# Kernel optimization log

Measured on AMD Instinct MI355X. Metric: run time of the kernel, lower is better.

The kernel has to match this reference:

```python
import jax, jax.numpy as jnp
import numpy as np

D_M, L_OBS, ALPHA, D_H, D_V, N_HEADS = 64, 256, 256, 256, 64, 8


def setup_inputs():
    key = jax.random.key(0)
    ks = jax.random.split(key, 18)
    x_ts = jax.random.normal(ks[0], (D_M, L_OBS), dtype=jnp.float32)
    t_raw = jax.random.uniform(ks[1], (D_M, L_OBS), dtype=jnp.float32) * ALPHA
    drop = jax.random.uniform(ks[2], (D_M, L_OBS)) < 0.5
    t_ts = jnp.where(drop, -1.0, t_raw)  # negative time == invalid observation
    global_means = jax.random.normal(ks[3], (D_M,), dtype=jnp.float32)
    s = 0.05
    return {
        'x_ts': x_ts, 't_ts': t_ts, 'global_means': global_means,
        'conv_w': jax.random.normal(ks[4], (D_H, D_M)) * s,
        'conv_b': jax.random.normal(ks[5], (D_H,)) * s,
        't2v_w': jax.random.normal(ks[6], (N_HEADS, D_V)),
        't2v_phi': jax.random.normal(ks[7], (N_HEADS, D_V)),
        'wq_w': jax.random.normal(ks[8], (N_HEADS, D_V, D_V)) * s,
        'wq_b': jax.random.normal(ks[9], (N_HEADS, D_V)) * s,
        'wk_w': jax.random.normal(ks[10], (N_HEADS, D_V, D_V)) * s,
        'wk_b': jax.random.normal(ks[11], (N_HEADS, D_V)) * s,
        'proj_w': jax.random.normal(ks[12], (D_H, N_HEADS)) * s,
        'proj_b': jax.random.normal(ks[13], (D_H,)) * s,
        'g1_w': jax.random.normal(ks[14], (D_H, 2 * D_H)) * s,
        'g1_b': jax.random.normal(ks[15], (D_H,)) * s,
        'g2_w': jax.random.normal(ks[16], (D_H, D_H)) * s,
        'g2_b': jax.random.normal(ks[17], (D_H,)) * s,
    }


def _time2vec(tau, w, phi):
    # tau [...], w/phi [H, D_V] -> [H, *tau.shape, D_V]; dim 0 linear, rest sin
    shp = (N_HEADS,) + (1,) * tau.ndim + (D_V,)
    full = w.reshape(shp) * tau[None, ..., None] + phi.reshape(shp)
    return jnp.concatenate([full[..., :1], jnp.sin(full[..., 1:])], axis=-1)


def _impute_row(x, t, gm):
    # ALPHA grid via int(time), then forward-fill starting from global mean.
    valid = (~jnp.isnan(x)) & (t >= 0)
    idx = t.astype(jnp.int32)  # truncation matches int(obs_time.item()) for t>=0
    inr = valid & (idx < ALPHA)
    seg = jnp.where(inr, idx, ALPHA)  # invalid obs go to dropped segment
    order = jnp.arange(L_OBS, dtype=jnp.int32)
    last = jax.ops.segment_max(jnp.where(inr, order, -1), seg,
                               num_segments=ALPHA + 1)[:ALPHA]
    present = last >= 0
    vals = x[jnp.clip(last, 0, L_OBS - 1)]          # value written to each slot
    pos = jnp.where(present, jnp.arange(ALPHA, dtype=jnp.int32), -1)
    lastpos = jax.lax.cummax(pos, axis=0)            # last observed slot <= t
    return jnp.where(lastpos >= 0, vals[jnp.clip(lastpos, 0, ALPHA - 1)], gm)


def _forward(x_ts, t_ts, global_means, conv_w, conv_b, t2v_w, t2v_phi,
             wq_w, wq_b, wk_w, wk_b, proj_w, proj_b, g1_w, g1_b, g2_w, g2_b):
    # --- imputation branch ---
    regular = jax.vmap(_impute_row)(x_ts, t_ts, global_means)  # [d_m, alpha]
    e_imp = (conv_w @ regular).T + conv_b                      # [alpha, d_h]
    # --- mTAND branch (masked attention over ragged observations) ---
    valid = (~jnp.isnan(x_ts)) & (t_ts >= 0)                   # [d_m, L]
    x_safe = jnp.where(valid, x_ts, 0.0)
    t_safe = jnp.where(valid, t_ts, 0.0)
    alpha_pts = jnp.arange(ALPHA, dtype=jnp.float32)
    theta_a = _time2vec(alpha_pts, t2v_w, t2v_phi)             # [H, alpha, d_v]
    q = jnp.einsum('had,hed->hae', theta_a, wq_w) + wq_b[:, None, :]
    theta_o = _time2vec(t_safe, t2v_w, t2v_phi)                # [H, d_m, L, d_v]
    k = jnp.einsum('hjld,hed->hjle', theta_o, wk_w) + wk_b[:, None, None, :]
    scores = jnp.einsum('hae,hjle->hjal', q, k) / np.float32(np.sqrt(D_V))
    scores = jnp.where(valid[None, :, None, :], scores, -1e9)  # exp underflows to 0
    attn = jax.nn.softmax(scores, axis=-1)                     # [H, d_m, alpha, L]
    # fully-invalid features: uniform attn * x_safe==0 -> zeros (matches torch)
    interp = jnp.einsum('hjal,jl->jah', attn, x_safe)          # [d_m, alpha, H]
    e_attn = (interp @ proj_w.T + proj_b).mean(axis=0)         # [alpha, d_h]
    # --- hidden_space gate ---
    concat = jnp.concatenate([e_imp, e_attn], axis=-1)         # [alpha, 2*d_h]
    g = jax.nn.sigmoid(jax.nn.relu(concat @ g1_w.T + g1_b) @ g2_w.T + g2_b)
    return g * e_imp + (1.0 - g) * e_attn                      # [alpha, d_h]


def reference(x_ts, t_ts, global_means, conv_w, conv_b, t2v_w, t2v_phi,
              wq_w, wq_b, wk_w, wk_b, proj_w, proj_b, g1_w, g1_b, g2_w, g2_b):
    return _forward(x_ts, t_ts, global_means, conv_w, conv_b, t2v_w, t2v_phi,
                    wq_w, wq_b, wk_w, wk_b, proj_w, proj_b, g1_w, g1_b, g2_w, g2_b)
```

## Files before the change

kernel.cpp:

```cpp
#include <hip/hip_runtime.h>

#define D_M     64
#define L_OBS   256
#define ALPHA   256
#define D_H     256
#define D_V     64
#define N_HEADS 8

typedef _Float16 half8 __attribute__((ext_vector_type(8)));
typedef float    f32x4 __attribute__((ext_vector_type(4)));

__global__ __launch_bounds__(256) void prep_kernel(
    const float* __restrict__ x_ts, const float* __restrict__ t_ts,
    const float* __restrict__ gm,
    const float* __restrict__ t2v_w, const float* __restrict__ t2v_phi,
    const float* __restrict__ wq_w, const float* __restrict__ wq_b,
    const float* __restrict__ wk_w,
    float* __restrict__ regular, float* __restrict__ QWbuf,
    float* __restrict__ QWabsG)
{
    const int tid = threadIdx.x;

    __shared__ int   last[ALPHA];
    __shared__ float vals[ALPHA];
    __shared__ int   wtot[4];
    __shared__ __align__(16) float wq_s[D_V][68];
    __shared__ __align__(16) float thA[16][68];
    __shared__ __align__(16) float QaT[16][68];

    if (blockIdx.x < D_M) {
        const int m  = blockIdx.x;
        const int l  = tid;
        const int wv = tid >> 6;
        const int ln = tid & 63;
        last[l] = -1;
        __syncthreads();
        float x = x_ts[m * L_OBS + l];
        float t = t_ts[m * L_OBS + l];
        bool valid = (x == x) && (t >= 0.0f);
        int idx = (int)t;
        if (valid && idx < ALPHA) atomicMax(&last[idx], l);
        __syncthreads();
        int li = last[l];
        vals[l] = (li >= 0) ? x_ts[m * L_OBS + li] : 0.0f;
        int p = (li >= 0) ? l : -1;
        #pragma unroll
        for (int s = 1; s < 64; s <<= 1) {
            int q = __shfl_up(p, s);
            if (ln >= s && q > p) p = q;
        }
        if (ln == 63) wtot[wv] = p;
        __syncthreads();
        int pre = -1;
        for (int w = 0; w < 4; w++)
            if (w < wv && wtot[w] > pre) pre = wtot[w];
        int lp = (pre > p) ? pre : p;
        regular[m * ALPHA + l] = (lp >= 0) ? vals[lp] : gm[m];
    } else {
        const int pb = blockIdx.x - D_M;
        const int h  = pb >> 4;
        const int a0 = (pb & 15) * 16;

        {
            const float4* w4 = (const float4*)(wq_w + h * D_V * D_V);
            #pragma unroll
            for (int i = 0; i < 4; i++) {
                int f = i * 256 + tid;
                float4 v = w4[f];
                int e = f >> 4, c = (f & 15) * 4;
                *(float4*)&wq_s[e][c] = v;
            }
        }
        {
            int al = tid >> 4, j0 = (tid & 15) * 4;
            float tv = (float)(a0 + al);
            #pragma unroll
            for (int j = 0; j < 4; j++) {
                int d = j0 + j;
                float f = t2v_w[h * D_V + d] * tv + t2v_phi[h * D_V + d];
                thA[al][d] = (d == 0) ? f : __sinf(f);
            }
        }
        __syncthreads();

        {
            const int e  = tid >> 2;
            const int ap = tid & 3;
            float accA[4] = {0.f, 0.f, 0.f, 0.f};
            const float4* wrow = (const float4*)&wq_s[e][0];
            #pragma unroll
            for (int j = 0; j < 16; j++) {
                float4 w = wrow[j];
                #pragma unroll
                for (int k = 0; k < 4; k++) {
                    float4 tv = *(const float4*)&thA[ap + 4 * k][j * 4];
                    accA[k] += w.x * tv.x + w.y * tv.y + w.z * tv.z + w.w * tv.w;
                }
            }
            float bq = wq_b[h * D_V + e];
            #pragma unroll
            for (int k = 0; k < 4; k++) QaT[ap + 4 * k][e] = accA[k] + bq;
        }
        __syncthreads();

        const int d  = tid >> 2;
        const int ap = tid & 3;
        float accB[4] = {0.f, 0.f, 0.f, 0.f};
        #pragma unroll 4
        for (int e4 = 0; e4 < 16; e4++) {
            const float* wkp = &wk_w[(h * D_V + e4 * 4) * D_V + d];
            float w0 = wkp[0];
            float w1 = wkp[D_V];
            float w2 = wkp[2 * D_V];
            float w3 = wkp[3 * D_V];
            #pragma unroll
            for (int k = 0; k < 4; k++) {
                float4 qv = *(const float4*)&QaT[ap + 4 * k][e4 * 4];
                accB[k] += qv.x * w0 + qv.y * w1 + qv.z * w2 + qv.w * w3;
            }
        }
        #pragma unroll
        for (int k = 0; k < 4; k++)
            QWbuf[h * D_V * ALPHA + d * ALPHA + a0 + ap + 4 * k] = accB[k];

        __syncthreads();
        #pragma unroll
        for (int k = 0; k < 4; k++)
            wq_s[d][ap + 4 * k] = (d == 0) ? 0.0f : fabsf(accB[k]);
        __syncthreads();
        if (tid < 16) {
            float s = 0.0f;
            #pragma unroll 8
            for (int dd = 0; dd < D_V; dd++) s += wq_s[dd][tid];
            QWabsG[h * ALPHA + a0 + tid] = s;
        }
    }
}

__global__ __launch_bounds__(256) void attn_mfma_kernel(
    const float* __restrict__ x_ts, const float* __restrict__ t_ts,
    const float* __restrict__ t2v_w, const float* __restrict__ t2v_phi,
    const float* __restrict__ QWbuf, const float* __restrict__ QWabsG,
    float* __restrict__ interp)
{
    const int ah  = blockIdx.x;
    const int m   = blockIdx.y;
    const int h   = blockIdx.z;
    const int tid = threadIdx.x;
    const int wv  = tid >> 6;
    const int ln  = tid & 63;
    const int lg  = ln >> 4;
    const int lc  = ln & 15;

    __shared__ float xc[L_OBS], tc[L_OBS];
    __shared__ float w_sh[D_V], phi_sh[D_V];
    __shared__ __align__(16) _Float16 hiB[2][2048];
    __shared__ __align__(16) _Float16 reB[2][2048];
    __shared__ float red_s[8];
    __shared__ int   cnt_s[4];

    xc[tid] = 0.0f;
    tc[tid] = 0.0f;
    float x = x_ts[m * L_OBS + tid];
    float t = t_ts[m * L_OBS + tid];
    bool  v = (x == x) && (t >= 0.0f);
    unsigned long long bal = __ballot(v);
    if (ln == 0) cnt_s[wv] = __popcll(bal);
    {
        float tmx = v ? t : -3.0e38f;
        float tmn = v ? t : 3.0e38f;
        #pragma unroll
        for (int s = 1; s < 64; s <<= 1) {
            tmx = fmaxf(tmx, __shfl_xor(tmx, s));
            tmn = fminf(tmn, __shfl_xor(tmn, s));
        }
        if (ln == 0) { red_s[wv] = tmx; red_s[4 + wv] = tmn; }
    }
    if (tid < D_V)          w_sh[tid]         = t2v_w[h * D_V + tid];
    else if (tid < 2 * D_V) phi_sh[tid - D_V] = t2v_phi[h * D_V + tid - D_V];
    __syncthreads();

    const int c0 = cnt_s[0], c1 = cnt_s[1], c2 = cnt_s[2], c3 = cnt_s[3];
    const int Lv = c0 + c1 + c2 + c3;
    {
        int base = (wv > 0 ? c0 : 0) + (wv > 1 ? c1 : 0) + (wv > 2 ? c2 : 0);
        unsigned long long lm = (1ull << ln) - 1ull;
        if (v) { int p = base + __popcll(bal & lm); xc[p] = x; tc[p] = t; }
    }

    const float tmaxv = fmaxf(fmaxf(red_s[0], red_s[1]), fmaxf(red_s[2], red_s[3]));
    const float tminv = fminf(fminf(red_s[4], red_s[5]), fminf(red_s[6], red_s[7]));
    const bool  anyv  = tmaxv > -1.0e37f;

    const float* __restrict__ QWh = QWbuf + h * D_V * ALPHA;
    const float w0 = w_sh[0], p0 = phi_sh[0];
    const float SCALE2 = 0.18033688011112042f;

    half8 ahf[2][2], arf[2][2];
    float qw0[2][4], c0b[2][4];
    #pragma unroll
    for (int at = 0; at < 2; at++) {
        const int abase = ah * 128 + wv * 32 + at * 16;
        const int arowA = abase + lc;
        #pragma unroll
        for (int kb = 0; kb < 2; kb++) {
            #pragma unroll
            for (int j = 0; j < 8; j++) {
                int d = 1 + kb * 32 + ((j >> 2) << 4) + (lg << 2) + (j & 3);
                float q = (d < D_V) ? QWh[d * ALPHA + arowA] : 0.0f;
                _Float16 qh = (_Float16)q;
                ahf[at][kb][j] = qh;
                arf[at][kb][j] = (_Float16)(q - (float)qh);
            }
        }
        const int arowD = abase + lg * 4;
        #pragma unroll
        for (int r = 0; r < 4; r++) {
            float q0 = QWh[arowD + r];
            qw0[at][r] = q0;
            float u = q0 * w0;
            float lin = q0 * p0 + fmaxf(u * tmaxv, u * tminv);
            c0b[at][r] = -(lin + QWabsG[h * ALPHA + arowD + r]);
        }
    }

    float ssum[2][4], axs[2][4];
    #pragma unroll
    for (int at = 0; at < 2; at++)
        #pragma unroll
        for (int r = 0; r < 4; r++) { ssum[at][r] = 0.0f; axs[at][r] = 0.0f; }

    const int wc  = tid >> 5;
    const int lcw = (tid >> 1) & 15;
    const int dB  = 1 + (wc >> 2) * 32 + (wc & 3) * 4 + ((tid & 1) << 4);

    auto write_frags = [&](int lt, int buf, int slot) {
        float tvw = tc[lt * 16 + lcw];
        float s0 = __sinf(fmaf(w_sh[(dB + 0) & 63], tvw, phi_sh[(dB + 0) & 63]));
        float s1 = __sinf(fmaf(w_sh[(dB + 1) & 63], tvw, phi_sh[(dB + 1) & 63]));
        float s2 = __sinf(fmaf(w_sh[(dB + 2) & 63], tvw, phi_sh[(dB + 2) & 63]));
        float s3 = __sinf(fmaf(w_sh[(dB + 3) & 63], tvw, phi_sh[(dB + 3) & 63]));
        union { _Float16 hv[4]; float2 f2; } hw, rw;
        hw.hv[0] = (_Float16)s0; hw.hv[1] = (_Float16)s1;
        hw.hv[2] = (_Float16)s2; hw.hv[3] = (_Float16)s3;
        rw.hv[0] = (_Float16)(s0 - (float)hw.hv[0]);
        rw.hv[1] = (_Float16)(s1 - (float)hw.hv[1]);
        rw.hv[2] = (_Float16)(s2 - (float)hw.hv[2]);
        rw.hv[3] = (_Float16)(s3 - (float)hw.hv[3]);
        *(float2*)&hiB[buf][slot * 1024 + tid * 4] = hw.f2;
        *(float2*)&reB[buf][slot * 1024 + tid * 4] = rw.f2;
    };

    const int nst  = (Lv + 15) >> 4;
    const int nreg = (nst + 1) >> 1;

    __syncthreads();
    write_frags(0, 0, 0);
    write_frags(1, 0, 1);
    __syncthreads();

    for (int rg = 0; rg < nreg; rg++) {
        const int cur = rg & 1;
        if (rg + 1 < nreg) {
            write_frags(2 * rg + 2, cur ^ 1, 0);
            write_frags(2 * rg + 3, cur ^ 1, 1);
        }
        #pragma unroll
        for (int s = 0; s < 2; s++) {
            const int st = 2 * rg + s;
            if (st >= nst) break;
            half8 bh[2], br[2];
            #pragma unroll
            for (int kb = 0; kb < 2; kb++) {
                int fi = s * 1024 + ((kb * 4 + lg) * 16 + lc) * 8;
                bh[kb] = *(const half8*)&hiB[cur][fi];
                br[kb] = *(const half8*)&reB[cur][fi];
            }
            const int l = st * 16 + lc;
            const float tv  = tc[l];
            const float xv  = xc[l];
            const float mkv = (l < Lv) ? 0.0f : -1.0e9f;
            const float tau = fmaf(w0, tv, p0);

            #pragma unroll
            for (int at = 0; at < 2; at++) {
                f32x4 acc;
                #pragma unroll
                for (int r = 0; r < 4; r++)
                    acc[r] = fmaf(qw0[at][r], tau, c0b[at][r]);
                #pragma unroll
                for (int kb = 0; kb < 2; kb++) {
                    acc = __builtin_amdgcn_mfma_f32_16x16x32_f16(ahf[at][kb], bh[kb], acc, 0, 0, 0);
                    acc = __builtin_amdgcn_mfma_f32_16x16x32_f16(ahf[at][kb], br[kb], acc, 0, 0, 0);
                    acc = __builtin_amdgcn_mfma_f32_16x16x32_f16(arf[at][kb], bh[kb], acc, 0, 0, 0);
                }
                #pragma unroll
                for (int r = 0; r < 4; r++) {
                    float p = __builtin_amdgcn_exp2f(fmaf(acc[r], SCALE2, mkv));
                    ssum[at][r] += p;
                    axs[at][r]   = fmaf(p, xv, axs[at][r]);
                }
            }
        }
        __syncthreads();
    }

    #pragma unroll
    for (int at = 0; at < 2; at++) {
        #pragma unroll
        for (int r = 0; r < 4; r++) {
            float S = ssum[at][r];
            float A = axs[at][r];
            S += __shfl_xor(S, 1); A += __shfl_xor(A, 1);
            S += __shfl_xor(S, 2); A += __shfl_xor(A, 2);
            S += __shfl_xor(S, 4); A += __shfl_xor(A, 4);
            S += __shfl_xor(S, 8); A += __shfl_xor(A, 8);
            if (lc == 0) {
                int a = ah * 128 + wv * 32 + at * 16 + lg * 4 + r;
                interp[a * (D_M * N_HEADS) + m * N_HEADS + h] =
                    anyv ? (A / S) : 0.0f;
            }
        }
    }
}

__global__ __launch_bounds__(256) void final_kernel(
    const float* __restrict__ regular, const float* __restrict__ interp,
    const float* __restrict__ conv_w, const float* __restrict__ conv_b,
    const float* __restrict__ proj_w, const float* __restrict__ proj_b,
    const float* __restrict__ g1_w, const float* __restrict__ g1_b,
    const float* __restrict__ g2_w, const float* __restrict__ g2_b,
    float* __restrict__ out)
{
    const int a = blockIdx.x;
    const int tid = threadIdx.x;
    __shared__ float isum_s[N_HEADS];
    __shared__ __align__(16) float col[D_M];
    __shared__ __align__(16) float c_s[2 * D_H];
    __shared__ __align__(16) float h_s[D_H];

    if (tid < 64) {
        const float4* i4 = (const float4*)&interp[a * (D_M * N_HEADS) + tid * 8];
        float4 v0 = i4[0], v1 = i4[1];
        float v[8] = {v0.x, v0.y, v0.z, v0.w, v1.x, v1.y, v1.z, v1.w};
        #pragma unroll
        for (int s = 1; s < 64; s <<= 1) {
            #pragma unroll
            for (int j = 0; j < 8; j++) v[j] += __shfl_xor(v[j], s);
        }
        if (tid == 0) {
            #pragma unroll
            for (int j = 0; j < 8; j++) isum_s[j] = v[j];
        }
    } else if (tid < 128) {
        col[tid - 64] = regular[(tid - 64) * ALPHA + a];
    }
    __syncthreads();

    float vattn;
    {
        const float4* p4 = (const float4*)&proj_w[tid * N_HEADS];
        float4 v0 = p4[0], v1 = p4[1];
        float sum = v0.x * isum_s[0] + v0.y * isum_s[1] + v0.z * isum_s[2]
                  + v0.w * isum_s[3] + v1.x * isum_s[4] + v1.y * isum_s[5]
                  + v1.z * isum_s[6] + v1.w * isum_s[7];
        vattn = proj_b[tid] + sum * (1.0f / 64.0f);
    }
    float vimp;
    {
        const float4* row = (const float4*)&conv_w[tid * D_M];
        const float4* c4  = (const float4*)col;
        float s0 = 0.f, s1 = 0.f, s2 = 0.f, s3 = 0.f;
        #pragma unroll
        for (int i = 0; i < D_M / 4; i++) {
            float4 r = row[i]; float4 c = c4[i];
            s0 += r.x * c.x; s1 += r.y * c.y; s2 += r.z * c.z; s3 += r.w * c.w;
        }
        vimp = conv_b[tid] + ((s0 + s1) + (s2 + s3));
    }
    c_s[tid]       = vimp;
    c_s[D_H + tid] = vattn;
    __syncthreads();

    {
        const float4* grow = (const float4*)&g1_w[tid * 2 * D_H];
        const float4* c4 = (const float4*)c_s;
        float s0 = 0.f, s1 = 0.f, s2 = 0.f, s3 = 0.f;
        #pragma unroll 8
        for (int i = 0; i < (2 * D_H) / 4; i++) {
            float4 g = grow[i]; float4 c = c4[i];
            s0 += g.x * c.x; s1 += g.y * c.y; s2 += g.z * c.z; s3 += g.w * c.w;
        }
        float hid = g1_b[tid] + ((s0 + s1) + (s2 + s3));
        h_s[tid] = fmaxf(hid, 0.0f);
    }
    __syncthreads();
    {
        const float4* grow = (const float4*)&g2_w[tid * D_H];
        const float4* h4 = (const float4*)h_s;
        float s0 = 0.f, s1 = 0.f, s2 = 0.f, s3 = 0.f;
        #pragma unroll 8
        for (int i = 0; i < D_H / 4; i++) {
            float4 g = grow[i]; float4 hh = h4[i];
            s0 += g.x * hh.x; s1 += g.y * hh.y; s2 += g.z * hh.z; s3 += g.w * hh.w;
        }
        float z = g2_b[tid] + ((s0 + s1) + (s2 + s3));
        float gate = 1.0f / (1.0f + __expf(-z));
        out[a * D_H + tid] = gate * vimp + (1.0f - gate) * vattn;
    }
}

extern "C" void kernel_launch(void* const* d_in, const int* in_sizes, int n_in,
                              void* d_out, int out_size, void* d_ws, size_t ws_size,
                              hipStream_t stream)
{
    (void)in_sizes; (void)n_in; (void)out_size; (void)ws_size;

    const float* x_ts    = (const float*)d_in[0];
    const float* t_ts    = (const float*)d_in[1];
    const float* gm      = (const float*)d_in[2];
    const float* conv_w  = (const float*)d_in[3];
    const float* conv_b  = (const float*)d_in[4];
    const float* t2v_w   = (const float*)d_in[5];
    const float* t2v_phi = (const float*)d_in[6];
    const float* wq_w    = (const float*)d_in[7];
    const float* wq_b    = (const float*)d_in[8];
    const float* wk_w    = (const float*)d_in[9];
    const float* proj_w  = (const float*)d_in[11];
    const float* proj_b  = (const float*)d_in[12];
    const float* g1_w    = (const float*)d_in[13];
    const float* g1_b    = (const float*)d_in[14];
    const float* g2_w    = (const float*)d_in[15];
    const float* g2_b    = (const float*)d_in[16];

    float* out = (float*)d_out;

    float* ws      = (float*)d_ws;
    float* regular = ws;
    float* QWbuf   = regular + D_M * ALPHA;
    float* interp  = QWbuf + N_HEADS * D_V * ALPHA;
    float* QWabs   = interp + ALPHA * D_M * N_HEADS;

    prep_kernel<<<D_M + 128, 256, 0, stream>>>(
        x_ts, t_ts, gm, t2v_w, t2v_phi, wq_w, wq_b, wk_w,
        regular, QWbuf, QWabs);
    attn_mfma_kernel<<<dim3(2, D_M, N_HEADS), 256, 0, stream>>>(
        x_ts, t_ts, t2v_w, t2v_phi, QWbuf, QWabs, interp);
    final_kernel<<<ALPHA, 256, 0, stream>>>(
        regular, interp, conv_w, conv_b, proj_w, proj_b,
        g1_w, g1_b, g2_w, g2_b, out);
}
```

Before: 52.72 us.

## Merge alpha-half blocks into one 512-thread block to share time2vec fragments

The attention kernel now launches one 512-thread block per (feature, head) instead of two 256-thread blocks split over alpha halves. Each block covers all 256 alpha rows with 8 waves. The sin-based key fragments for each observation tile are computed once and shared by all rows, rather than recomputed in each half-block. Fragment staging is also parallelised: the two 16-column slots are written by the two thread halves in one pass. In exchange there are half as many blocks, and each block uses more threads and registers, which may reduce occupancy or latency hiding.

```diff
diff --git a/kernel.cpp b/kernel.cpp
--- a/kernel.cpp
+++ b/kernel.cpp
@@ -137,15 +137,14 @@
     }
 }
 
-__global__ __launch_bounds__(256) void attn_mfma_kernel(
+__global__ __launch_bounds__(512) void attn_mfma_kernel(
     const float* __restrict__ x_ts, const float* __restrict__ t_ts,
     const float* __restrict__ t2v_w, const float* __restrict__ t2v_phi,
     const float* __restrict__ QWbuf, const float* __restrict__ QWabsG,
     float* __restrict__ interp)
 {
-    const int ah  = blockIdx.x;
-    const int m   = blockIdx.y;
-    const int h   = blockIdx.z;
+    const int m   = blockIdx.x;
+    const int h   = blockIdx.y;
     const int tid = threadIdx.x;
     const int wv  = tid >> 6;
     const int ln  = tid & 63;
@@ -159,14 +158,20 @@
     __shared__ float red_s[8];
     __shared__ int   cnt_s[4];
 
-    xc[tid] = 0.0f;
-    tc[tid] = 0.0f;
-    float x = x_ts[m * L_OBS + tid];
-    float t = t_ts[m * L_OBS + tid];
-    bool  v = (x == x) && (t >= 0.0f);
-    unsigned long long bal = __ballot(v);
-    if (ln == 0) cnt_s[wv] = __popcll(bal);
-    {
+    if (tid < L_OBS) { xc[tid] = 0.0f; tc[tid] = 0.0f; }
+    if (tid < D_V)                      w_sh[tid]          = t2v_w[h * D_V + tid];
+    else if (tid >= 256 && tid < 256 + D_V)
+        phi_sh[tid - 256] = t2v_phi[h * D_V + tid - 256];
+
+    float x = 0.0f, t = 0.0f;
+    bool  v = false;
+    unsigned long long bal = 0;
+    if (tid < L_OBS) {
+        x = x_ts[m * L_OBS + tid];
+        t = t_ts[m * L_OBS + tid];
+        v = (x == x) && (t >= 0.0f);
+        bal = __ballot(v);
+        if (ln == 0) cnt_s[wv] = __popcll(bal);
         float tmx = v ? t : -3.0e38f;
         float tmn = v ? t : 3.0e38f;
         #pragma unroll
@@ -176,16 +181,15 @@
         }
         if (ln == 0) { red_s[wv] = tmx; red_s[4 + wv] = tmn; }
     }
-    if (tid < D_V)          w_sh[tid]         = t2v_w[h * D_V + tid];
-    else if (tid < 2 * D_V) phi_sh[tid - D_V] = t2v_phi[h * D_V + tid - D_V];
     __syncthreads();
 
     const int c0 = cnt_s[0], c1 = cnt_s[1], c2 = cnt_s[2], c3 = cnt_s[3];
     const int Lv = c0 + c1 + c2 + c3;
-    {
+    if (tid < L_OBS && v) {
         int base = (wv > 0 ? c0 : 0) + (wv > 1 ? c1 : 0) + (wv > 2 ? c2 : 0);
         unsigned long long lm = (1ull << ln) - 1ull;
-        if (v) { int p = base + __popcll(bal & lm); xc[p] = x; tc[p] = t; }
+        int p = base + __popcll(bal & lm);
+        xc[p] = x; tc[p] = t;
     }
 
     const float tmaxv = fmaxf(fmaxf(red_s[0], red_s[1]), fmaxf(red_s[2], red_s[3]));
@@ -200,7 +204,7 @@
     float qw0[2][4], c0b[2][4];
     #pragma unroll
     for (int at = 0; at < 2; at++) {
-        const int abase = ah * 128 + wv * 32 + at * 16;
+        const int abase = wv * 32 + at * 16;
         const int arowA = abase + lc;
         #pragma unroll
         for (int kb = 0; kb < 2; kb++) {
@@ -230,11 +234,14 @@
         #pragma unroll
         for (int r = 0; r < 4; r++) { ssum[at][r] = 0.0f; axs[at][r] = 0.0f; }
 
-    const int wc  = tid >> 5;
-    const int lcw = (tid >> 1) & 15;
-    const int dB  = 1 + (wc >> 2) * 32 + (wc & 3) * 4 + ((tid & 1) << 4);
-
-    auto write_frags = [&](int lt, int buf, int slot) {
+    const int slot = tid >> 8;
+    const int t2   = tid & 255;
+    const int wc   = t2 >> 5;
+    const int lcw  = (t2 >> 1) & 15;
+    const int dB   = 1 + (wc >> 2) * 32 + (wc & 3) * 4 + ((t2 & 1) << 4);
+
+    auto write2 = [&](int lt0, int buf) {
+        int lt = lt0 + slot;
         float tvw = tc[lt * 16 + lcw];
         float s0 = __sinf(fmaf(w_sh[(dB + 0) & 63], tvw, phi_sh[(dB + 0) & 63]));
         float s1 = __sinf(fmaf(w_sh[(dB + 1) & 63], tvw, phi_sh[(dB + 1) & 63]));
@@ -247,24 +254,20 @@
         rw.hv[1] = (_Float16)(s1 - (float)hw.hv[1]);
         rw.hv[2] = (_Float16)(s2 - (float)hw.hv[2]);
         rw.hv[3] = (_Float16)(s3 - (float)hw.hv[3]);
-        *(float2*)&hiB[buf][slot * 1024 + tid * 4] = hw.f2;
-        *(float2*)&reB[buf][slot * 1024 + tid * 4] = rw.f2;
+        *(float2*)&hiB[buf][slot * 1024 + t2 * 4] = hw.f2;
+        *(float2*)&reB[buf][slot * 1024 + t2 * 4] = rw.f2;
     };
 
     const int nst  = (Lv + 15) >> 4;
     const int nreg = (nst + 1) >> 1;
 
     __syncthreads();
-    write_frags(0, 0, 0);
-    write_frags(1, 0, 1);
+    write2(0, 0);
     __syncthreads();
 
     for (int rg = 0; rg < nreg; rg++) {
         const int cur = rg & 1;
-        if (rg + 1 < nreg) {
-            write_frags(2 * rg + 2, cur ^ 1, 0);
-            write_frags(2 * rg + 3, cur ^ 1, 1);
-        }
+        if (rg + 1 < nreg) write2(2 * rg + 2, cur ^ 1);
         #pragma unroll
         for (int s = 0; s < 2; s++) {
             const int st = 2 * rg + s;
@@ -316,7 +319,7 @@
             S += __shfl_xor(S, 4); A += __shfl_xor(A, 4);
             S += __shfl_xor(S, 8); A += __shfl_xor(A, 8);
             if (lc == 0) {
-                int a = ah * 128 + wv * 32 + at * 16 + lg * 4 + r;
+                int a = wv * 32 + at * 16 + lg * 4 + r;
                 interp[a * (D_M * N_HEADS) + m * N_HEADS + h] =
                     anyv ? (A / S) : 0.0f;
             }
@@ -444,7 +447,7 @@
     prep_kernel<<<D_M + 128, 256, 0, stream>>>(
         x_ts, t_ts, gm, t2v_w, t2v_phi, wq_w, wq_b, wk_w,
         regular, QWbuf, QWabs);
-    attn_mfma_kernel<<<dim3(2, D_M, N_HEADS), 256, 0, stream>>>(
+    attn_mfma_kernel<<<dim3(D_M, N_HEADS), 512, 0, stream>>>(
         x_ts, t_ts, t2v_w, t2v_phi, QWbuf, QWabs, interp);
     final_kernel<<<ALPHA, 256, 0, stream>>>(
         regular, interp, conv_w, conv_b, proj_w, proj_b,
```

New measurement: 51.61 us. 1.02x faster.
